# Kernel tuning notes

Hardware: AMD Instinct MI355X
Metric: run time of the kernel (lower is better)

The kernel has to match this reference:

```python
import jax, jax.numpy as jnp
import numpy as np

HIDDEN = 256
NUM_NODES = 500000
NUM_GRAPHS = 8192
EPS = 1e-16


def setup_inputs() -> dict:
    key = jax.random.key(0)
    ks = jax.random.split(key, 8)
    x = jax.random.normal(ks[0], (NUM_NODES, HIDDEN), dtype=jnp.float32)
    batch = jnp.sort(jax.random.randint(ks[1], (NUM_NODES,), 0, NUM_GRAPHS, dtype=jnp.int64))
    h2 = HIDDEN // 2
    # gate_nn: Linear(H, H/2) -> SiLU -> Linear(H/2, 1)
    w_g1 = jax.random.normal(ks[2], (HIDDEN, h2), dtype=jnp.float32) / np.sqrt(HIDDEN)
    b_g1 = jnp.zeros((h2,), dtype=jnp.float32)
    w_g2 = jax.random.normal(ks[3], (h2, 1), dtype=jnp.float32) / np.sqrt(h2)
    b_g2 = jnp.zeros((1,), dtype=jnp.float32)
    # value_nn: Linear(H, H) -> SiLU
    w_v = jax.random.normal(ks[4], (HIDDEN, HIDDEN), dtype=jnp.float32) / np.sqrt(HIDDEN)
    b_v = jnp.zeros((HIDDEN,), dtype=jnp.float32)
    return {"x": x, "batch": batch, "w_g1": w_g1, "b_g1": b_g1,
            "w_g2": w_g2, "b_g2": b_g2, "w_v": w_v, "b_v": b_v}


def reference(x, batch, w_g1, b_g1, w_g2, b_g2, w_v, b_v):
    batch = batch.astype(jnp.int32)
    # gate scores [N]
    g_hid = jax.nn.silu(x @ w_g1 + b_g1)                      # [N, H/2]
    gates = (g_hid @ w_g2 + b_g2)[:, 0]                      # [N]
    # segment-wise stable softmax over nodes of each graph
    seg_max = jax.ops.segment_max(gates, batch, num_segments=NUM_GRAPHS)
    e = jnp.exp(gates - seg_max[batch])                       # [N]
    seg_sum = jax.ops.segment_sum(e, batch, num_segments=NUM_GRAPHS)
    attn = e / (seg_sum[batch] + EPS)                         # [N]
    # value transform and weighted scatter-add pooling
    values = jax.nn.silu(x @ w_v + b_v)                       # [N, H]
    out = jax.ops.segment_sum(attn[:, None] * values, batch, num_segments=NUM_GRAPHS)
    return out                                                # [G, H]
```

## Files before the change

### kernel.cpp

```cpp
#include <hip/hip_runtime.h>
#include <hip/hip_bf16.h>

#define HIDDEN 256
#define H2 128
#define NCOLS 384
#define NUM_GRAPHS 8192
#define GPB 2
#define PPB 8
#define NBLK (NUM_GRAPHS / GPB / PPB)

typedef short bf16x8 __attribute__((ext_vector_type(8)));
typedef float f32x4 __attribute__((ext_vector_type(4)));

__device__ __forceinline__ unsigned short f32_bf16_rne(float f) {
  union { float f; unsigned int u; } v; v.f = f;
  unsigned int u = v.u;
  unsigned int lsb = (u >> 16) & 1u;
  u += 0x7fffu + lsb;
  return (unsigned short)(u >> 16);
}

__device__ __forceinline__ float silu_f(float h) {
  return h / (1.0f + __expf(-h));
}

__global__ void seg_starts_kernel(const int* __restrict__ batch,
                                  int* __restrict__ seg, int N) {
  int i = blockIdx.x * blockDim.x + threadIdx.x;
  if (i >= N) return;
  int cur = batch[i];
  int prev = (i == 0) ? -1 : batch[i - 1];
  for (int g = prev + 1; g <= cur; ++g) seg[g] = i;
  if (i == N - 1)
    for (int g = cur + 1; g <= NUM_GRAPHS; ++g) seg[g] = N;
}

__global__ void convert_w_kernel(const float* __restrict__ w_g1,
                                 const float* __restrict__ w_v,
                                 unsigned short* __restrict__ Wt2) {
  int idx = blockIdx.x * blockDim.x + threadIdx.x;
  int j  = idx & 7;
  int n  = (idx >> 3) % NCOLS;
  int kc = idx / (NCOLS * 8);
  int k  = kc * 8 + j;
  float v = (n < H2) ? w_g1[k * H2 + n] : w_v[k * HIDDEN + (n - H2)];
  Wt2[idx] = f32_bf16_rne(v);
}

__launch_bounds__(512, 2)
__global__ void attn_readout_kernel(
    const float* __restrict__ x,
    const float* __restrict__ b_g1,
    const float* __restrict__ w_g2,
    const float* __restrict__ b_g2,
    const float* __restrict__ b_v,
    const unsigned short* __restrict__ Wt2,
    const int* __restrict__ seg,
    float* __restrict__ out)
{
  __shared__ unsigned short As[2][64 * 264];
  __shared__ float gate_part[8][64];
  __shared__ float es[64];
  __shared__ float denom_s[2];

  const int tid  = threadIdx.x;
  const int w    = tid >> 6;
  const int lane = tid & 63;
  const int l15  = lane & 15;
  const int quad = lane >> 4;

  bf16x8 Bg[8], Bv0[8], Bv1[8];
#pragma unroll
  for (int c = 0; c < 8; ++c) {
    int kc = c * 4 + quad;
    const unsigned short* kb = Wt2 + (((size_t)kc * NCOLS) << 3);
    Bg[c]  = *(const bf16x8*)(kb + ((w * 16 + l15) << 3));
    Bv0[c] = *(const bf16x8*)(kb + ((128 + w * 16 + l15) << 3));
    Bv1[c] = *(const bf16x8*)(kb + ((256 + w * 16 + l15) << 3));
  }
  const float bg1 = b_g1[w * 16 + l15];
  const float wg2 = w_g2[w * 16 + l15];
  const float bv0 = b_v[w * 16 + l15];
  const float bv1 = b_v[128 + w * 16 + l15];
  const float bg2 = b_g2[0];

  for (int pp = 0; pp < PPB; ++pp) {
    const int g0      = (blockIdx.x * PPB + pp) * GPB;
    const int node_lo = seg[g0];
    const int split   = seg[g0 + 1];
    const int node_hi = seg[g0 + 2];

    float vg0t0 = 0.f, vg0t1 = .0f, vg1t0 = 0.f, vg1t1 = 0.f;
    float d0 = 0.f, d1 = 0.f;

    if (node_lo < node_hi) {
#pragma unroll
      for (int i = 0; i < 8; ++i) {
        int v = i * 512 + tid, row = v >> 6, c4 = v & 63;
        int node = node_lo + row;
        f32x4 val = (f32x4){0.f, 0.f, 0.f, 0.f};
        if (node < node_hi)
          val = __builtin_nontemporal_load(
              (const f32x4*)(x + ((size_t)node << 8) + (c4 << 2)));
        ushort4 u;
        u.x = f32_bf16_rne(val[0]); u.y = f32_bf16_rne(val[1]);
        u.z = f32_bf16_rne(val[2]); u.w = f32_bf16_rne(val[3]);
        *(ushort4*)&As[0][row * 264 + (c4 << 2)] = u;
      }
    }
    __syncthreads();

    int cur = 0;
    for (int node0 = node_lo; node0 < node_hi; node0 += 64, cur ^= 1) {
      const int  next0     = node0 + 64;
      const bool have_next = (next0 < node_hi);

      f32x4 sv[8];
      if (have_next) {
#pragma unroll
        for (int i = 0; i < 8; ++i) {
          int v = i * 512 + tid, row = v >> 6, c4 = v & 63;
          int node = next0 + row;
          sv[i] = (f32x4){0.f, 0.f, 0.f, 0.f};
          if (node < node_hi)
            sv[i] = __builtin_nontemporal_load(
                (const f32x4*)(x + ((size_t)node << 8) + (c4 << 2)));
        }
      }
      __builtin_amdgcn_sched_barrier(0);

      {
        f32x4 accg[4];
#pragma unroll
        for (int mt = 0; mt < 4; ++mt) accg[mt] = (f32x4){0.f, 0.f, 0.f, 0.f};
#pragma unroll
        for (int c = 0; c < 8; ++c) {
          bf16x8 a[4];
#pragma unroll
          for (int mt = 0; mt < 4; ++mt)
            a[mt] = *(const bf16x8*)&As[cur][(mt * 16 + l15) * 264 + c * 32 + quad * 8];
#pragma unroll
          for (int mt = 0; mt < 4; ++mt)
            accg[mt] = __builtin_amdgcn_mfma_f32_16x16x32_bf16(
                a[mt], Bg[c], accg[mt], 0, 0, 0);
        }
        float p[4][4];
#pragma unroll
        for (int mt = 0; mt < 4; ++mt)
#pragma unroll
          for (int r = 0; r < 4; ++r)
            p[mt][r] = silu_f(accg[mt][r] + bg1) * wg2;
#pragma unroll
        for (int off = 1; off < 16; off <<= 1)
#pragma unroll
          for (int mt = 0; mt < 4; ++mt)
#pragma unroll
            for (int r = 0; r < 4; ++r)
              p[mt][r] += __shfl_xor(p[mt][r], off, 64);
        if (l15 == 0)
#pragma unroll
          for (int mt = 0; mt < 4; ++mt)
#pragma unroll
            for (int r = 0; r < 4; ++r)
              gate_part[w][mt * 16 + quad * 4 + r] = p[mt][r];
      }
      __syncthreads();

      if (tid < 64) {
        int row = tid, node = node0 + row;
        float e = 0.f;
        if (node < node_hi) {
          float g = bg2;
#pragma unroll
          for (int ww = 0; ww < 8; ++ww) g += gate_part[ww][row];
          e = __expf(g);
          if (node < split) d0 += e; else d1 += e;
        }
        es[row] = e;
      }
      __syncthreads();

      {
        f32x4 accv[4][2];
#pragma unroll
        for (int mt = 0; mt < 4; ++mt) {
          accv[mt][0] = (f32x4){0.f, 0.f, 0.f, 0.f};
          accv[mt][1] = (f32x4){0.f, 0.f, 0.f, 0.f};
        }
#pragma unroll
        for (int c = 0; c < 8; ++c) {
          bf16x8 a[4];
#pragma unroll
          for (int mt = 0; mt < 4; ++mt)
            a[mt] = *(const bf16x8*)&As[cur][(mt * 16 + l15) * 264 + c * 32 + quad * 8];
#pragma unroll
          for (int mt = 0; mt < 4; ++mt) {
            accv[mt][0] = __builtin_amdgcn_mfma_f32_16x16x32_bf16(
                a[mt], Bv0[c], accv[mt][0], 0, 0, 0);
            accv[mt][1] = __builtin_amdgcn_mfma_f32_16x16x32_bf16(
                a[mt], Bv1[c], accv[mt][1], 0, 0, 0);
          }
        }
#pragma unroll
        for (int mt = 0; mt < 4; ++mt)
#pragma unroll
          for (int r = 0; r < 4; ++r) {
            int row  = mt * 16 + quad * 4 + r;
            int node = node0 + row;
            float e  = es[row];
            float se0 = (node < split) ? e : 0.f;
            float se1 = e - se0;
            float s0 = silu_f(accv[mt][0][r] + bv0);
            float s1 = silu_f(accv[mt][1][r] + bv1);
            vg0t0 += se0 * s0; vg0t1 += se0 * s1;
            vg1t0 += se1 * s0; vg1t1 += se1 * s1;
          }
      }

      if (have_next) {
#pragma unroll
        for (int i = 0; i < 8; ++i) {
          int v = i * 512 + tid, row = v >> 6, c4 = v & 63;
          ushort4 u;
          u.x = f32_bf16_rne(sv[i][0]); u.y = f32_bf16_rne(sv[i][1]);
          u.z = f32_bf16_rne(sv[i][2]); u.w = f32_bf16_rne(sv[i][3]);
          *(ushort4*)&As[cur ^ 1][row * 264 + (c4 << 2)] = u;
        }
      }
      __syncthreads();
    }

    vg0t0 += __shfl_xor(vg0t0, 16, 64); vg0t0 += __shfl_xor(vg0t0, 32, 64);
    vg0t1 += __shfl_xor(vg0t1, 16, 64); vg0t1 += __shfl_xor(vg0t1, 32, 64);
    vg1t0 += __shfl_xor(vg1t0, 16, 64); vg1t0 += __shfl_xor(vg1t0, 32, 64);
    vg1t1 += __shfl_xor(vg1t1, 16, 64); vg1t1 += __shfl_xor(vg1t1, 32, 64);
    if (w == 0) {
#pragma unroll
      for (int off = 1; off < 64; off <<= 1) {
        d0 += __shfl_xor(d0, off, 64);
        d1 += __shfl_xor(d1, off, 64);
      }
      if (lane == 0) { denom_s[0] = d0; denom_s[1] = d1; }
    }
    __syncthreads();

    if (quad == 0) {
      float inv0 = 1.0f / (denom_s[0] + 1e-16f);
      float inv1 = 1.0f / (denom_s[1] + 1e-16f);
      out[(size_t)g0 * 256 + w * 16 + l15]             = vg0t0 * inv0;
      out[(size_t)g0 * 256 + 128 + w * 16 + l15]       = vg0t1 * inv0;
      out[(size_t)(g0 + 1) * 256 + w * 16 + l15]       = vg1t0 * inv1;
      out[(size_t)(g0 + 1) * 256 + 128 + w * 16 + l15] = vg1t1 * inv1;
    }
    __syncthreads();
  }
}

extern "C" void kernel_launch(void* const* d_in, const int* in_sizes, int n_in,
                              void* d_out, int out_size, void* d_ws, size_t ws_size,
                              hipStream_t stream) {
  const float* x    = (const float*)d_in[0];
  const int*   batch= (const int*)d_in[1];
  const float* w_g1 = (const float*)d_in[2];
  const float* b_g1 = (const float*)d_in[3];
  const float* w_g2 = (const float*)d_in[4];
  const float* b_g2 = (const float*)d_in[5];
  const float* w_v  = (const float*)d_in[6];
  const float* b_v  = (const float*)d_in[7];
  float* out = (float*)d_out;
  const int N = in_sizes[0] / HIDDEN;

  unsigned short* Wt2 = (unsigned short*)d_ws;
  int* seg = (int*)((char*)d_ws + (size_t)NCOLS * HIDDEN * sizeof(unsigned short));

  seg_starts_kernel<<<(N + 255) / 256, 256, 0, stream>>>(batch, seg, N);
  convert_w_kernel<<<(NCOLS * HIDDEN) / 256, 256, 0, stream>>>(w_g1, w_v, Wt2);
  attn_readout_kernel<<<NBLK, 512, 0, stream>>>(
      x, b_g1, w_g2, b_g2, b_v, Wt2, seg, out);
}
```

Baseline: 907.3 us.

## Fuse gate and value MFMAs, prefetch across graph pairs, cut barriers per tile

Gate and value GEMMs now run in one MFMA loop, so each tile needs a single barrier instead of three. Every wave computes the softmax denominators itself, which removes the end-of-pair barriers and shared-memory broadcast. The prefetch of the next 64-node tile now reaches across graph-pair boundaries, so the first tile of the next pair is already staged. It also adds packed bf16 conversion via v_cvt_pk_bf16_f32, DPP row reductions, s_setprio around the MFMAs, and halves PPB, doubling the block count. Costs are more live accumulator registers, double-buffered gate/es shared arrays, and redundant per-wave exp work.

```diff
diff --git a/kernel.cpp b/kernel.cpp
--- a/kernel.cpp
+++ b/kernel.cpp
@@ -6,22 +6,33 @@
 #define NCOLS 384
 #define NUM_GRAPHS 8192
 #define GPB 2
-#define PPB 8
+#define PPB 4
 #define NBLK (NUM_GRAPHS / GPB / PPB)
 
 typedef short bf16x8 __attribute__((ext_vector_type(8)));
 typedef float f32x4 __attribute__((ext_vector_type(4)));
 
-__device__ __forceinline__ unsigned short f32_bf16_rne(float f) {
-  union { float f; unsigned int u; } v; v.f = f;
-  unsigned int u = v.u;
-  unsigned int lsb = (u >> 16) & 1u;
-  u += 0x7fffu + lsb;
-  return (unsigned short)(u >> 16);
-}
-
 __device__ __forceinline__ float silu_f(float h) {
   return h / (1.0f + __expf(-h));
+}
+
+__device__ __forceinline__ unsigned int cvt_pk_bf16(float a, float b) {
+  unsigned int r;
+  asm volatile("v_cvt_pk_bf16_f32 %0, %1, %2" : "=v"(r) : "v"(a), "v"(b));
+  return r;
+}
+
+__device__ __forceinline__ float dpp_sum16(float v) {
+  int t;
+  t = __builtin_amdgcn_update_dpp(0, __builtin_bit_cast(int, v), 0x111, 0xf, 0xf, true);
+  v += __builtin_bit_cast(float, t);
+  t = __builtin_amdgcn_update_dpp(0, __builtin_bit_cast(int, v), 0x112, 0xf, 0xf, true);
+  v += __builtin_bit_cast(float, t);
+  t = __builtin_amdgcn_update_dpp(0, __builtin_bit_cast(int, v), 0x114, 0xf, 0xf, true);
+  v += __builtin_bit_cast(float, t);
+  t = __builtin_amdgcn_update_dpp(0, __builtin_bit_cast(int, v), 0x118, 0xf, 0xf, true);
+  v += __builtin_bit_cast(float, t);
+  return v;
 }
 
 __global__ void seg_starts_kernel(const int* __restrict__ batch,
@@ -44,7 +55,9 @@
   int kc = idx / (NCOLS * 8);
   int k  = kc * 8 + j;
   float v = (n < H2) ? w_g1[k * H2 + n] : w_v[k * HIDDEN + (n - H2)];
-  Wt2[idx] = f32_bf16_rne(v);
+  union { float f; unsigned int u; } c; c.f = v;
+  unsigned int u = c.u; u += 0x7fffu + ((u >> 16) & 1u);
+  Wt2[idx] = (unsigned short)(u >> 16);
 }
 
 __launch_bounds__(512, 2)
@@ -59,9 +72,8 @@
     float* __restrict__ out)
 {
   __shared__ unsigned short As[2][64 * 264];
-  __shared__ float gate_part[8][64];
-  __shared__ float es[64];
-  __shared__ float denom_s[2];
+  __shared__ float gate_part[2][8][64];
+  __shared__ float es2[2][64];
 
   const int tid  = threadIdx.x;
   const int w    = tid >> 6;
@@ -84,55 +96,66 @@
   const float bv1 = b_v[128 + w * 16 + l15];
   const float bg2 = b_g2[0];
 
+  const int gbase = blockIdx.x * (PPB * GPB);
+  int  cur    = 0;
+  bool staged = false;
+
   for (int pp = 0; pp < PPB; ++pp) {
-    const int g0      = (blockIdx.x * PPB + pp) * GPB;
+    const int g0      = gbase + pp * GPB;
     const int node_lo = seg[g0];
     const int split   = seg[g0 + 1];
     const int node_hi = seg[g0 + 2];
-
-    float vg0t0 = 0.f, vg0t1 = .0f, vg1t0 = 0.f, vg1t1 = 0.f;
+    const int hi2     = (pp + 1 < PPB) ? seg[g0 + 4] : node_hi;
+
+    float vg0t0 = 0.f, vg0t1 = 0.f, vg1t0 = 0.f, vg1t1 = 0.f;
     float d0 = 0.f, d1 = 0.f;
 
     if (node_lo < node_hi) {
-#pragma unroll
-      for (int i = 0; i < 8; ++i) {
-        int v = i * 512 + tid, row = v >> 6, c4 = v & 63;
-        int node = node_lo + row;
-        f32x4 val = (f32x4){0.f, 0.f, 0.f, 0.f};
-        if (node < node_hi)
-          val = __builtin_nontemporal_load(
-              (const f32x4*)(x + ((size_t)node << 8) + (c4 << 2)));
-        ushort4 u;
-        u.x = f32_bf16_rne(val[0]); u.y = f32_bf16_rne(val[1]);
-        u.z = f32_bf16_rne(val[2]); u.w = f32_bf16_rne(val[3]);
-        *(ushort4*)&As[0][row * 264 + (c4 << 2)] = u;
-      }
-    }
-    __syncthreads();
-
-    int cur = 0;
-    for (int node0 = node_lo; node0 < node_hi; node0 += 64, cur ^= 1) {
-      const int  next0     = node0 + 64;
-      const bool have_next = (next0 < node_hi);
-
-      f32x4 sv[8];
-      if (have_next) {
+      if (!staged) {
 #pragma unroll
         for (int i = 0; i < 8; ++i) {
           int v = i * 512 + tid, row = v >> 6, c4 = v & 63;
-          int node = next0 + row;
-          sv[i] = (f32x4){0.f, 0.f, 0.f, 0.f};
+          int node = node_lo + row;
+          f32x4 val = (f32x4){0.f, 0.f, 0.f, 0.f};
           if (node < node_hi)
-            sv[i] = __builtin_nontemporal_load(
+            val = __builtin_nontemporal_load(
                 (const f32x4*)(x + ((size_t)node << 8) + (c4 << 2)));
-        }
+          unsigned int lo = cvt_pk_bf16(val[0], val[1]);
+          unsigned int hi = cvt_pk_bf16(val[2], val[3]);
+          *(uint2*)&As[cur][row * 264 + (c4 << 2)] = make_uint2(lo, hi);
+        }
+        __syncthreads();
       }
-      __builtin_amdgcn_sched_barrier(0);
-
-      {
+
+      for (int node0 = node_lo; node0 < node_hi; node0 += 64) {
+        const bool in_pair   = (node0 + 64 < node_hi);
+        const int  nstart    = in_pair ? node0 + 64 : node_hi;
+        const int  nlimit    = in_pair ? node_hi    : hi2;
+        const bool have_next = nstart < nlimit;
+
+        f32x4 sv[8];
+        if (have_next) {
+#pragma unroll
+          for (int i = 0; i < 8; ++i) {
+            int v = i * 512 + tid, row = v >> 6, c4 = v & 63;
+            int node = nstart + row;
+            sv[i] = (f32x4){0.f, 0.f, 0.f, 0.f};
+            if (node < nlimit)
+              sv[i] = __builtin_nontemporal_load(
+                  (const f32x4*)(x + ((size_t)node << 8) + (c4 << 2)));
+          }
+        }
+        __builtin_amdgcn_sched_barrier(0);
+
         f32x4 accg[4];
-#pragma unroll
-        for (int mt = 0; mt < 4; ++mt) accg[mt] = (f32x4){0.f, 0.f, 0.f, 0.f};
+        f32x4 accv[4][2];
+#pragma unroll
+        for (int mt = 0; mt < 4; ++mt) {
+          accg[mt]    = (f32x4){0.f, 0.f, 0.f, 0.f};
+          accv[mt][0] = (f32x4){0.f, 0.f, 0.f, 0.f};
+          accv[mt][1] = (f32x4){0.f, 0.f, 0.f, 0.f};
+        }
+        __builtin_amdgcn_s_setprio(1);
 #pragma unroll
         for (int c = 0; c < 8; ++c) {
           bf16x8 a[4];
@@ -140,74 +163,58 @@
           for (int mt = 0; mt < 4; ++mt)
             a[mt] = *(const bf16x8*)&As[cur][(mt * 16 + l15) * 264 + c * 32 + quad * 8];
 #pragma unroll
-          for (int mt = 0; mt < 4; ++mt)
-            accg[mt] = __builtin_amdgcn_mfma_f32_16x16x32_bf16(
-                a[mt], Bg[c], accg[mt], 0, 0, 0);
-        }
-        float p[4][4];
-#pragma unroll
-        for (int mt = 0; mt < 4; ++mt)
-#pragma unroll
-          for (int r = 0; r < 4; ++r)
-            p[mt][r] = silu_f(accg[mt][r] + bg1) * wg2;
-#pragma unroll
-        for (int off = 1; off < 16; off <<= 1)
-#pragma unroll
-          for (int mt = 0; mt < 4; ++mt)
-#pragma unroll
-            for (int r = 0; r < 4; ++r)
-              p[mt][r] += __shfl_xor(p[mt][r], off, 64);
-        if (l15 == 0)
-#pragma unroll
-          for (int mt = 0; mt < 4; ++mt)
-#pragma unroll
-            for (int r = 0; r < 4; ++r)
-              gate_part[w][mt * 16 + quad * 4 + r] = p[mt][r];
-      }
-      __syncthreads();
-
-      if (tid < 64) {
-        int row = tid, node = node0 + row;
-        float e = 0.f;
-        if (node < node_hi) {
-          float g = bg2;
-#pragma unroll
-          for (int ww = 0; ww < 8; ++ww) g += gate_part[ww][row];
-          e = __expf(g);
-          if (node < split) d0 += e; else d1 += e;
-        }
-        es[row] = e;
-      }
-      __syncthreads();
-
-      {
-        f32x4 accv[4][2];
-#pragma unroll
-        for (int mt = 0; mt < 4; ++mt) {
-          accv[mt][0] = (f32x4){0.f, 0.f, 0.f, 0.f};
-          accv[mt][1] = (f32x4){0.f, 0.f, 0.f, 0.f};
-        }
-#pragma unroll
-        for (int c = 0; c < 8; ++c) {
-          bf16x8 a[4];
-#pragma unroll
-          for (int mt = 0; mt < 4; ++mt)
-            a[mt] = *(const bf16x8*)&As[cur][(mt * 16 + l15) * 264 + c * 32 + quad * 8];
-#pragma unroll
           for (int mt = 0; mt < 4; ++mt) {
+            accg[mt]    = __builtin_amdgcn_mfma_f32_16x16x32_bf16(
+                a[mt], Bg[c],  accg[mt],    0, 0, 0);
             accv[mt][0] = __builtin_amdgcn_mfma_f32_16x16x32_bf16(
                 a[mt], Bv0[c], accv[mt][0], 0, 0, 0);
             accv[mt][1] = __builtin_amdgcn_mfma_f32_16x16x32_bf16(
                 a[mt], Bv1[c], accv[mt][1], 0, 0, 0);
           }
         }
+        __builtin_amdgcn_s_setprio(0);
+
+#pragma unroll
+        for (int mt = 0; mt < 4; ++mt)
+#pragma unroll
+          for (int r = 0; r < 4; ++r) {
+            float p = silu_f(accg[mt][r] + bg1) * wg2;
+            p = dpp_sum16(p);
+            if (l15 == 15)
+              gate_part[cur][w][mt * 16 + quad * 4 + r] = p;
+          }
+
+        if (have_next) {
+#pragma unroll
+          for (int i = 0; i < 8; ++i) {
+            int v = i * 512 + tid, row = v >> 6, c4 = v & 63;
+            unsigned int lo = cvt_pk_bf16(sv[i][0], sv[i][1]);
+            unsigned int hi = cvt_pk_bf16(sv[i][2], sv[i][3]);
+            *(uint2*)&As[cur ^ 1][row * 264 + (c4 << 2)] = make_uint2(lo, hi);
+          }
+        }
+
+        __syncthreads();
+
+        {
+          int node = node0 + lane;
+          float g = bg2;
+#pragma unroll
+          for (int ww = 0; ww < 8; ++ww) g += gate_part[cur][ww][lane];
+          float e = (node < node_hi) ? __expf(g) : 0.f;
+          es2[cur][lane] = e;
+          float se0 = (node < split) ? e : 0.f;
+          d0 += se0;
+          d1 += e - se0;
+        }
+
 #pragma unroll
         for (int mt = 0; mt < 4; ++mt)
 #pragma unroll
           for (int r = 0; r < 4; ++r) {
             int row  = mt * 16 + quad * 4 + r;
             int node = node0 + row;
-            float e  = es[row];
+            float e  = es2[cur][row];
             float se0 = (node < split) ? e : 0.f;
             float se1 = e - se0;
             float s0 = silu_f(accv[mt][0][r] + bv0);
@@ -215,44 +222,29 @@
             vg0t0 += se0 * s0; vg0t1 += se0 * s1;
             vg1t0 += se1 * s0; vg1t1 += se1 * s1;
           }
+
+        staged = have_next && !in_pair;
+        cur ^= 1;
       }
-
-      if (have_next) {
-#pragma unroll
-        for (int i = 0; i < 8; ++i) {
-          int v = i * 512 + tid, row = v >> 6, c4 = v & 63;
-          ushort4 u;
-          u.x = f32_bf16_rne(sv[i][0]); u.y = f32_bf16_rne(sv[i][1]);
-          u.z = f32_bf16_rne(sv[i][2]); u.w = f32_bf16_rne(sv[i][3]);
-          *(ushort4*)&As[cur ^ 1][row * 264 + (c4 << 2)] = u;
-        }
-      }
-      __syncthreads();
     }
 
     vg0t0 += __shfl_xor(vg0t0, 16, 64); vg0t0 += __shfl_xor(vg0t0, 32, 64);
     vg0t1 += __shfl_xor(vg0t1, 16, 64); vg0t1 += __shfl_xor(vg0t1, 32, 64);
     vg1t0 += __shfl_xor(vg1t0, 16, 64); vg1t0 += __shfl_xor(vg1t0, 32, 64);
     vg1t1 += __shfl_xor(vg1t1, 16, 64); vg1t1 += __shfl_xor(vg1t1, 32, 64);
-    if (w == 0) {
-#pragma unroll
-      for (int off = 1; off < 64; off <<= 1) {
-        d0 += __shfl_xor(d0, off, 64);
-        d1 += __shfl_xor(d1, off, 64);
-      }
-      if (lane == 0) { denom_s[0] = d0; denom_s[1] = d1; }
+#pragma unroll
+    for (int off = 1; off < 64; off <<= 1) {
+      d0 += __shfl_xor(d0, off, 64);
+      d1 += __shfl_xor(d1, off, 64);
     }
-    __syncthreads();
-
     if (quad == 0) {
-      float inv0 = 1.0f / (denom_s[0] + 1e-16f);
-      float inv1 = 1.0f / (denom_s[1] + 1e-16f);
+      float inv0 = 1.0f / (d0 + 1e-16f);
+      float inv1 = 1.0f / (d1 + 1e-16f);
       out[(size_t)g0 * 256 + w * 16 + l15]             = vg0t0 * inv0;
       out[(size_t)g0 * 256 + 128 + w * 16 + l15]       = vg0t1 * inv0;
       out[(size_t)(g0 + 1) * 256 + w * 16 + l15]       = vg1t0 * inv1;
       out[(size_t)(g0 + 1) * 256 + 128 + w * 16 + l15] = vg1t1 * inv1;
     }
-    __syncthreads();
   }
 }
 
```

Result: faster. 865.8 us (-4.6%).
